# Kernel tuning notes

Measured on AMD Instinct MI355X. Metric: run time of the kernel, lower is better.

The kernel has to match this reference:

```python
import jax, jax.numpy as jnp
import numpy as np

B, T, L, D, H = 4, 8, 197, 512, 8
DK = D // H
SIM_TH = 0.0
N = T * (L - 1)  # 1568 local tokens

def _ln(x, g, b, eps=1e-5):
    x32 = x.astype(jnp.float32)
    m = jnp.mean(x32, axis=-1, keepdims=True)
    v = jnp.mean((x32 - m) ** 2, axis=-1, keepdims=True)
    return (((x32 - m) * jax.lax.rsqrt(v + eps)) * g + b).astype(x.dtype)

def _qgelu(x):
    return x * jax.nn.sigmoid(1.702 * x)

def _mha(x, w_in, b_in, w_out, b_out):
    # torch nn.MultiheadAttention, x: [S, Bt, D] (seq-first)
    S, Bt, _ = x.shape
    qkv = x @ w_in.T + b_in
    q, k, v = jnp.split(qkv, 3, axis=-1)
    q = q.reshape(S, Bt, H, DK); k = k.reshape(S, Bt, H, DK); v = v.reshape(S, Bt, H, DK)
    scores = jnp.einsum('sbhd,tbhd->bhst', q, k) / jnp.sqrt(jnp.asarray(DK, x.dtype))
    p = jax.nn.softmax(scores, axis=-1)
    o = jnp.einsum('bhst,tbhd->sbhd', p, v).reshape(S, Bt, D)
    return o @ w_out.T + b_out

def _resblock(x, ln1g, ln1b, inw, inb, outw, outb, ln2g, ln2b, fcw, fcb, pw, pb):
    x = x + _mha(_ln(x, ln1g, ln1b), inw, inb, outw, outb)
    h = _qgelu(_ln(x, ln2g, ln2b) @ fcw.T + fcb)
    return x + h @ pw.T + pb

def _build_graph(x, g_mask):
    xd = jax.lax.stop_gradient(x)  # matches x.detach()
    xn = xd / jnp.maximum(jnp.linalg.norm(xd, axis=-1, keepdims=True), 1e-12)
    sim = jnp.einsum('bnd,bmd->bnm', xn, xn)
    adj = jnp.where(sim < SIM_TH, 0.0, sim)
    return adj * g_mask  # t != 1 branch

def _graph_attn(x, mask, wq, bq, wk, bk, wv, bv, wo, bo):
    Bb, Nn, _ = x.shape
    def heads(a):
        return a.reshape(Bb, Nn, H, DK).transpose(0, 2, 1, 3)
    Q = heads(x @ wq.T + bq); K = heads(x @ wk.T + bk); V = heads(x @ wv.T + bv)
    scores = jnp.einsum('bhnd,bhmd->bhnm', Q, K) / jnp.sqrt(jnp.asarray(DK, x.dtype))
    m = mask[:, None]  # [b,1,N,N]
    scores = jnp.where(m == 0, -jnp.inf, scores * m)  # scores*mask then masked_fill(mask==0,-inf)
    p = jax.nn.softmax(scores, axis=-1)
    o = jnp.einsum('bhnm,bhmd->bhnd', p, V).transpose(0, 2, 1, 3).reshape(Bb, Nn, D)
    return o @ wo.T + bo

def _forward(x, proj_w, proj_b,
             m_ln1g, m_ln1b, m_inw, m_inb, m_outw, m_outb,
             m_ln2g, m_ln2b, m_fcw, m_fcb, m_pw, m_pb,
             g_wq, g_bq, g_wk, g_bk, g_wv, g_bv, g_wo, g_bo,
             ln1g, ln1b, a_inw, a_inb, a_outw, a_outb,
             ln2g, ln2b, fcw, fcb, pw, pb, g_mask):
    b, t, l, d = x.shape
    x = x @ proj_w.T + proj_b
    glob = x[:, :, 0, :].transpose(1, 0, 2)  # [t,b,d]
    msg = (m_ln1g, m_ln1b, m_inw, m_inb, m_outw, m_outb, m_ln2g, m_ln2b, m_fcw, m_fcb, m_pw, m_pb)
    glob = _resblock(glob, *msg)
    glob = _resblock(glob, *msg)  # message_attn applied twice (shared weights)
    glob = glob.reshape(1, t, b, d)
    loc = x[:, :, 1:, :].reshape(b, t * (l - 1), d)
    gm = _build_graph(loc, g_mask)
    loc = _graph_attn(loc, gm, g_wq, g_bq, g_wk, g_bk, g_wv, g_bv, g_wo, g_bo)
    loc = loc.reshape(b, t, l - 1, d).transpose(2, 1, 0, 3)  # [l-1,t,b,d]
    y = jnp.concatenate([glob, loc], axis=0).reshape(l, t * b, d)
    y = y + _mha(_ln(y, ln1g, ln1b), a_inw, a_inb, a_outw, a_outb)
    y = y + _qgelu(_ln(y, ln2g, ln2b) @ fcw.T + fcb) @ pw.T + pb
    return y.reshape(l, t, b, d).transpose(2, 1, 0, 3)  # [b,t,l,d]

def setup_inputs() -> dict:
    key = jax.random.key(0)
    ks = jax.random.split(key, 64)
    s = 0.02
    def w(i, shape):
        return jax.random.normal(ks[i], shape, jnp.float32) * s
    ones = jnp.ones((D,), jnp.float32); zeros = jnp.zeros((D,), jnp.float32)
    gm = (jax.random.uniform(ks[60], (N, N)) < 0.5).astype(jnp.float32)
    gm = gm.at[jnp.arange(N), jnp.arange(N)].set(1.0)  # keep self-edges so no row is fully masked
    return dict(
        x=jax.random.normal(ks[0], (B, T, L, D), jnp.float32),
        proj_w=w(1, (D, D)), proj_b=jnp.zeros((D,), jnp.float32),
        m_ln1g=ones, m_ln1b=zeros,
        m_inw=w(2, (3 * D, D)), m_inb=jnp.zeros((3 * D,), jnp.float32),
        m_outw=w(3, (D, D)), m_outb=zeros,
        m_ln2g=ones, m_ln2b=zeros,
        m_fcw=w(4, (4 * D, D)), m_fcb=jnp.zeros((4 * D,), jnp.float32),
        m_pw=w(5, (D, 4 * D)), m_pb=zeros,
        g_wq=w(6, (D, D)), g_bq=zeros, g_wk=w(7, (D, D)), g_bk=zeros,
        g_wv=w(8, (D, D)), g_bv=zeros, g_wo=w(9, (D, D)), g_bo=zeros,
        ln1g=ones, ln1b=zeros,
        a_inw=w(10, (3 * D, D)), a_inb=jnp.zeros((3 * D,), jnp.float32),
        a_outw=w(11, (D, D)), a_outb=zeros,
        ln2g=ones, ln2b=zeros,
        fcw=w(12, (4 * D, D)), fcb=jnp.zeros((4 * D,), jnp.float32),
        pw=w(13, (D, 4 * D)), pb=zeros,
        g_mask=gm,
    )

def reference(x, proj_w, proj_b, m_ln1g, m_ln1b, m_inw, m_inb, m_outw, m_outb,
              m_ln2g, m_ln2b, m_fcw, m_fcb, m_pw, m_pb,
              g_wq, g_bq, g_wk, g_bk, g_wv, g_bv, g_wo, g_bo,
              ln1g, ln1b, a_inw, a_inb, a_outw, a_outb,
              ln2g, ln2b, fcw, fcb, pw, pb, g_mask):
    return _forward(x, proj_w, proj_b, m_ln1g, m_ln1b, m_inw, m_inb, m_outw, m_outb,
                    m_ln2g, m_ln2b, m_fcw, m_fcb, m_pw, m_pb,
                    g_wq, g_bq, g_wk, g_bk, g_wv, g_bv, g_wo, g_bo,
                    ln1g, ln1b, a_inw, a_inb, a_outw, a_outb,
                    ln2g, ln2b, fcw, fcb, pw, pb, g_mask)
```

## Files before the change

kernel.cpp:

```cpp
#include <hip/hip_runtime.h>
#include <hip/hip_bf16.h>

typedef unsigned short u16;
typedef __attribute__((ext_vector_type(8))) short bf16x8;
typedef __attribute__((ext_vector_type(4))) float f32x4;

#define FINF __builtin_huge_valf()

static __device__ __forceinline__ float bf2f(u16 v){ union{unsigned u; float f;} c; c.u = ((unsigned)v)<<16; return c.f; }
static __device__ __forceinline__ u16 f2bf(float f){ union{__hip_bfloat16 h; u16 u;} c; c.h = __float2bfloat16(f); return c.u; }
static __device__ __forceinline__ bf16x8 scale8(bf16x8 v, float s){
  bf16x8 o;
  #pragma unroll
  for (int e=0;e<8;e++) o[e] = (short)f2bf(bf2f((u16)v[e])*s);
  return o;
}

static __device__ __forceinline__ void gload16(const void* g, void* l){
  __builtin_amdgcn_global_load_lds(
      (const __attribute__((address_space(1))) void*)g,
      (__attribute__((address_space(3))) void*)l, 16, 0, 0);
}

#define WAIT_VM0()   { asm volatile("s_waitcnt vmcnt(0)" ::: "memory"); __builtin_amdgcn_sched_barrier(0); }
#define BARRIER()    { __builtin_amdgcn_sched_barrier(0); __builtin_amdgcn_s_barrier(); __builtin_amdgcn_sched_barrier(0); }

struct CvtArgs {
  const float* src[14];
  u16* dst[14];
  int n[14];
};
__global__ __launch_bounds__(256) void cvt_multi(CvtArgs a){
  int seg = blockIdx.y;
  const float* s = a.src[seg]; u16* d = a.dst[seg]; int n = a.n[seg];
  for (int i = (blockIdx.x*256 + threadIdx.x)*4; i < n; i += gridDim.x*256*4){
    float4 v = *(const float4*)(s + i);
    ushort4 o = { f2bf(v.x), f2bf(v.y), f2bf(v.z), f2bf(v.w) };
    *(ushort4*)(d + i) = o;
  }
}

__global__ __launch_bounds__(256) void concat_bias(const float* a, const float* b, const float* c, float* o){
  int i = blockIdx.x*256 + threadIdx.x;
  o[i] = i < 512 ? a[i] : (i < 1024 ? b[i-512] : c[i-1024]);
}

template<int BM, int EPI, int MW>
__global__ __launch_bounds__(256,MW) void gemm_nt(
    const u16* __restrict__ A, const u16* __restrict__ Bw,
    const float* __restrict__ bias, const float* aux, void* out,
    int M, int Nn, int K, int ldc, long aBatch, long bBatch, long cBatch)
{
  constexpr int MI = BM/32;
  constexpr int WSPAN = BM/2;
  __shared__ __align__(16) u16 a_lds[2*BM*64];
  __shared__ __align__(16) u16 b_lds[2*128*64];
  const int z = blockIdx.z;
  const u16* Az = A + (long)z*aBatch;
  const u16* Bz = Bw + (long)z*bBatch;
  const int n0 = blockIdx.x*128, m0 = blockIdx.y*BM;
  const int t = threadIdx.x, lane = t & 63, wave = t >> 6;
  const int wr = wave >> 1, wc = wave & 1;
  const int r = lane & 15, kq = lane >> 4;

  const int srow = t >> 3;
  const int scol = ((t&7)*8) ^ ((srow&7)<<3);
  int rowA[MI], rowB[4];
  #pragma unroll
  for (int i=0;i<MI;i++){ int ga = m0 + i*32 + srow; rowA[i] = ga < M ? ga : M-1; }
  #pragma unroll
  for (int i=0;i<4;i++){ int gb = n0 + i*32 + srow; rowB[i] = gb < Nn ? gb : Nn-1; }

  f32x4 acc[MI][4] = {};
  const int nkt = K >> 6;

  auto STAGE = [&](int kt, int buf){
    const long koff = (long)kt*64 + scol;
    #pragma unroll
    for (int i=0;i<MI;i++)
      gload16(Az + (long)rowA[i]*K + koff, (char*)a_lds + buf*(BM*128) + i*4096 + wave*1024);
    #pragma unroll
    for (int i=0;i<4;i++)
      gload16(Bz + (long)rowB[i]*K + koff, (char*)b_lds + buf*16384 + i*4096 + wave*1024);
  };

  STAGE(0,0);
  WAIT_VM0(); BARRIER();
  for (int kt=0; kt<nkt; kt++){
    const int cur = kt&1;
    if (kt+1 < nkt) STAGE(kt+1, cur^1);
    const u16* al = a_lds + cur*BM*64;
    const u16* bl = b_lds + cur*8192;
    #pragma unroll
    for (int kk=0; kk<2; kk++){
      bf16x8 af[MI], bfr[4];
      #pragma unroll
      for (int i=0;i<MI;i++){
        int rw = wr*WSPAN + i*16 + r;
        af[i] = *(const bf16x8*)&al[rw*64 + ((kk*32 + kq*8) ^ ((rw&7)<<3))];
      }
      #pragma unroll
      for (int j=0;j<4;j++){
        int rw = wc*64 + j*16 + r;
        bfr[j] = *(const bf16x8*)&bl[rw*64 + ((kk*32 + kq*8) ^ ((rw&7)<<3))];
      }
      #pragma unroll
      for (int i=0;i<MI;i++)
        #pragma unroll
        for (int j=0;j<4;j++)
          acc[i][j] = __builtin_amdgcn_mfma_f32_16x16x32_bf16(af[i], bfr[j], acc[i][j], 0,0,0);
    }
    WAIT_VM0(); BARRIER();
  }

  #pragma unroll
  for (int i=0;i<MI;i++){
    #pragma unroll
    for (int j=0;j<4;j++){
      int gcol = n0 + wc*64 + j*16 + r;
      if (gcol >= Nn) continue;
      float bv = bias ? bias[gcol] : 0.f;
      #pragma unroll
      for (int rr=0; rr<4; rr++){
        int grow = m0 + wr*WSPAN + i*16 + kq*4 + rr;
        if (grow >= M) continue;
        float v = acc[i][j][rr] + bv;
        if constexpr (EPI==0){
          ((float*)out)[(long)z*cBatch + (long)grow*ldc + gcol] = v;
        } else if constexpr (EPI==1){
          ((u16*)out)[(long)z*cBatch + (long)grow*ldc + gcol] = f2bf(v);
        } else if constexpr (EPI==2){
          long idx = (long)z*cBatch + (long)grow*ldc + gcol;
          ((float*)out)[idx] = aux[idx] + v;
        } else if constexpr (EPI==3){
          float g = v / (1.f + __expf(-1.702f*v));
          ((u16*)out)[(long)z*cBatch + (long)grow*ldc + gcol] = f2bf(g);
        } else if constexpr (EPI==4){
          float adj = v < 0.f ? 0.f : v;
          float gmv = aux[(long)grow*Nn + gcol];
          ((u16*)out)[(long)z*cBatch + (long)grow*ldc + gcol] = f2bf(adj*gmv);
        } else if constexpr (EPI==5){
          int b = grow/1568, n = grow%1568, tt = n/196, lp = n%196;
          int yrow = (1+lp)*32 + tt*4 + b;
          ((float*)out)[(long)yrow*ldc + gcol] = v;
        } else if constexpr (EPI==6){
          long idx = (long)grow*ldc + gcol;
          int l = grow>>5, rb = grow&31, tt = rb>>2, bb = rb&3;
          ((float*)out)[((long)((bb*8+tt)*197) + l)*512 + gcol] = aux[idx] + v;
        }
      }
    }
  }
}

__global__ __launch_bounds__(256) void transpose_v(
    const u16* __restrict__ src, u16* __restrict__ vt,
    int nrows, long zofs, long nofs, int vcol0, int outld)
{
  __shared__ u16 tile[64][66];
  const int t = threadIdx.x;
  const int nt = blockIdx.x, h = blockIdx.y, z = blockIdx.z;
  const int n0 = nt*64;
  const int rlo = t>>3, c0 = (t&7)*8;
  #pragma unroll
  for (int i=0;i<2;i++){
    int nl = i*32 + rlo;
    int n = n0 + nl; int nc = n < nrows ? n : nrows-1;
    const u16* s = src + (long)z*zofs + (long)nc*nofs + vcol0 + h*64 + c0;
    uint4 v = *(const uint4*)s;
    bool dead = n >= nrows;
    #pragma unroll
    for (int e=0;e<8;e++) tile[nl][c0+e] = dead ? (u16)0 : ((const u16*)&v)[e];
  }
  __syncthreads();
  #pragma unroll
  for (int i=0;i<2;i++){
    int d = i*32 + rlo;
    u16 tmp[8];
    #pragma unroll
    for (int e=0;e<8;e++) tmp[e] = tile[c0+e][d];
    int ncol = n0 + c0;
    if (ncol + 8 <= outld){
      u16* dst = vt + ((long)((z*8+h)*64 + d))*outld + ncol;
      *(uint4*)dst = *(uint4*)tmp;
    }
  }
}

template<bool MASKED>
__global__ __launch_bounds__(256,3) void flash4(
    const u16* __restrict__ QKV, const u16* __restrict__ VT,
    const u16* __restrict__ gmask, u16* __restrict__ Out,
    int nq, int nk, int nqb, long qBatch, long qRow,
    long oBatch, long oRow, long gmBatch, int vtld)
{
  __shared__ __align__(16) u16 k_lds[2*4096];
  __shared__ __align__(16) u16 p_lds[4][2][1024];
  int h, z, qb;
  if constexpr (MASKED){
    int id = blockIdx.x;
    int a = id>>6, c = id&7; h = (id>>3)&7;
    int G = a*8 + c;
    if (G >= 4*nqb) return;
    z = G / nqb; qb = G % nqb;
  } else {
    qb = blockIdx.x; h = blockIdx.y; z = blockIdx.z;
  }
  const int t = threadIdx.x, lane = t&63, wave = t>>6;
  const int r = lane&15, kq = lane>>4;
  const u16* Qb = QKV + (long)z*qBatch + h*64;
  const u16* Kb = Qb + 512;
  const u16* Vt = VT + (long)(z*8+h)*64*vtld;
  const int qt0 = qb*128;

  int qi[2], qc[2];
  bf16x8 qf[2][2];
  const u16* Gq[2];
  #pragma unroll
  for (int qt=0; qt<2; qt++){
    qi[qt] = qt0 + qt*64 + wave*16 + r;
    qc[qt] = qi[qt] < nq ? qi[qt] : nq-1;
    const u16* qp = Qb + (long)qc[qt]*qRow + kq*8;
    qf[qt][0] = scale8(*(const bf16x8*)qp, 0.125f);
    qf[qt][1] = scale8(*(const bf16x8*)(qp+32), 0.125f);
    Gq[qt] = MASKED ? (gmask + (long)z*gmBatch + (long)qc[qt]*nk) : nullptr;
  }

  const int srow = t>>3;
  const int scol = ((t&7)*8) ^ ((srow&7)<<3);

  auto stage_k = [&](int kt, int buf){
    #pragma unroll
    for (int i=0;i<2;i++){
      int j = kt*64 + i*32 + srow; if (j > nk-1) j = nk-1;
      gload16(Kb + (long)j*qRow + scol, (char*)k_lds + buf*8192 + i*4096 + wave*1024);
    }
  };

  bf16x8 ONES;
  #pragma unroll
  for (int e=0;e<8;e++) ONES[e] = (short)0x3F80;

  float m_[2] = {-FINF,-FINF};
  f32x4 o_[2][4] = {};  f32x4 l_[2] = {};

  const int nkt = (nk + 63) >> 6;
  stage_k(0,0);
  __syncthreads();
  for (int kt=0; kt<nkt; kt++){
    const int cur = kt&1;
    if (kt+1 < nkt) stage_k(kt+1, cur^1);

    uint4 vfr[2][4];
    #pragma unroll
    for (int c=0;c<2;c++)
      #pragma unroll
      for (int j=0;j<4;j++)
        vfr[c][j] = *(const uint4*)(Vt + (long)(j*16+r)*vtld + kt*64 + c*32 + kq*8);

    const u16* kl = k_lds + cur*4096;
    #pragma unroll
    for (int qt=0; qt<2; qt++){
      ushort4 gv[4];
      if constexpr (MASKED){
        #pragma unroll
        for (int sub=0;sub<4;sub++)
          gv[sub] = *(const ushort4*)(Gq[qt] + kt*64 + sub*16 + kq*4);
      }

      float p[4][4];
      #pragma unroll
      for (int sub=0; sub<4; sub++){
        int rw = sub*16 + r; int sw = (rw&7)<<3;
        bf16x8 kf0 = *(const bf16x8*)&kl[rw*64 + ((kq*8) ^ sw)];
        bf16x8 kf1 = *(const bf16x8*)&kl[rw*64 + ((32 + kq*8) ^ sw)];
        f32x4 sc = {};
        sc = __builtin_amdgcn_mfma_f32_16x16x32_bf16(kf0, qf[qt][0], sc, 0,0,0);
        sc = __builtin_amdgcn_mfma_f32_16x16x32_bf16(kf1, qf[qt][1], sc, 0,0,0);
        #pragma unroll
        for (int rr=0;rr<4;rr++){
          float sv = sc[rr];
          int key = kt*64 + sub*16 + kq*4 + rr;
          if constexpr (MASKED){
            u16 g = ((const u16*)&gv[sub])[rr];
            sv = (g == 0 || key >= nk) ? -FINF : sv * bf2f(g);
          } else {
            if (key >= nk) sv = -FINF;
          }
          p[sub][rr] = sv;
        }
      }

      float mx;
      { float a0 = fmaxf(fmaxf(p[0][0],p[0][1]), fmaxf(p[0][2],p[0][3]));
        float a1 = fmaxf(fmaxf(p[1][0],p[1][1]), fmaxf(p[1][2],p[1][3]));
        float a2 = fmaxf(fmaxf(p[2][0],p[2][1]), fmaxf(p[2][2],p[2][3]));
        float a3 = fmaxf(fmaxf(p[3][0],p[3][1]), fmaxf(p[3][2],p[3][3]));
        mx = fmaxf(fmaxf(a0,a1), fmaxf(a2,a3)); }
      mx = fmaxf(mx, __shfl_xor(mx, 16));
      mx = fmaxf(mx, __shfl_xor(mx, 32));
      float mnew = fmaxf(m_[qt], mx);
      if (__any(mnew > m_[qt])){
        float fac = (m_[qt] == -FINF) ? 0.f : __expf(m_[qt] - mnew);
        #pragma unroll
        for (int j=0;j<4;j++){ o_[qt][j][0]*=fac; o_[qt][j][1]*=fac; o_[qt][j][2]*=fac; o_[qt][j][3]*=fac; }
        l_[qt][0]*=fac; l_[qt][1]*=fac; l_[qt][2]*=fac; l_[qt][3]*=fac;
        m_[qt] = mnew;
      }
      mnew = m_[qt];

      #pragma unroll
      for (int sub=0;sub<4;sub++){
        float e0 = (p[sub][0] == -FINF) ? 0.f : __expf(p[sub][0] - mnew);
        float e1 = (p[sub][1] == -FINF) ? 0.f : __expf(p[sub][1] - mnew);
        float e2 = (p[sub][2] == -FINF) ? 0.f : __expf(p[sub][2] - mnew);
        float e3 = (p[sub][3] == -FINF) ? 0.f : __expf(p[sub][3] - mnew);
        unsigned u0, u1;
        asm volatile("v_cvt_pk_bf16_f32 %0, %1, %2" : "=v"(u0) : "v"(e0), "v"(e1));
        asm volatile("v_cvt_pk_bf16_f32 %0, %1, %2" : "=v"(u1) : "v"(e2), "v"(e3));
        uint2 w; w.x = u0; w.y = u1;
        int idx = r*64 + ((sub*16 + kq*4) ^ ((r&7)<<3));
        *(uint2*)&p_lds[wave][qt][idx] = w;
      }

      #pragma unroll
      for (int c=0;c<2;c++){
        bf16x8 pf = *(const bf16x8*)&p_lds[wave][qt][r*64 + ((c*32 + kq*8) ^ ((r&7)<<3))];
        #pragma unroll
        for (int j=0;j<4;j++){
          bf16x8 vf = *(const bf16x8*)&vfr[c][j];
          o_[qt][j] = __builtin_amdgcn_mfma_f32_16x16x32_bf16(vf, pf, o_[qt][j], 0,0,0);
        }
        l_[qt] = __builtin_amdgcn_mfma_f32_16x16x32_bf16(ONES, pf, l_[qt], 0,0,0);
      }
    }
    __syncthreads();
  }

  #pragma unroll
  for (int qt=0; qt<2; qt++){
    float inv = l_[qt][0] > 0.f ? 1.f/l_[qt][0] : 0.f;
    if (qi[qt] < nq){
      #pragma unroll
      for (int j=0;j<4;j++){
        ushort4 ov = { f2bf(o_[qt][j][0]*inv), f2bf(o_[qt][j][1]*inv),
                       f2bf(o_[qt][j][2]*inv), f2bf(o_[qt][j][3]*inv) };
        *(ushort4*)(Out + (long)z*oBatch + (long)qi[qt]*oRow + h*64 + j*16 + kq*4) = ov;
      }
    }
  }
}

__global__ __launch_bounds__(256) void ln_rows(const float* __restrict__ in,
    const float* __restrict__ g, const float* __restrict__ b, u16* __restrict__ out, int rows)
{
  int wave = threadIdx.x >> 6, lane = threadIdx.x & 63;
  int row = blockIdx.x*4 + wave;
  if (row >= rows) return;
  const float4* x = (const float4*)(in + (long)row*512);
  float4 v0 = x[lane], v1 = x[lane+64];
  float s  = v0.x+v0.y+v0.z+v0.w + v1.x+v1.y+v1.z+v1.w;
  float ss = v0.x*v0.x+v0.y*v0.y+v0.z*v0.z+v0.w*v0.w + v1.x*v1.x+v1.y*v1.y+v1.z*v1.z+v1.w*v1.w;
  #pragma unroll
  for (int d=1; d<64; d<<=1){ s += __shfl_xor(s,d); ss += __shfl_xor(ss,d); }
  float mean = s * (1.f/512.f);
  float var = ss * (1.f/512.f) - mean*mean;
  float rs = rsqrtf(var + 1e-5f);
  const float4* gg = (const float4*)g; const float4* bb = (const float4*)b;
  float4 g0 = gg[lane], g1 = gg[lane+64], b0 = bb[lane], b1 = bb[lane+64];
  u16* o = out + (long)row*512;
  ushort4 o0 = { f2bf((v0.x-mean)*rs*g0.x + b0.x), f2bf((v0.y-mean)*rs*g0.y + b0.y),
                 f2bf((v0.z-mean)*rs*g0.z + b0.z), f2bf((v0.w-mean)*rs*g0.w + b0.w) };
  ushort4 o1 = { f2bf((v1.x-mean)*rs*g1.x + b1.x), f2bf((v1.y-mean)*rs*g1.y + b1.y),
                 f2bf((v1.z-mean)*rs*g1.z + b1.z), f2bf((v1.w-mean)*rs*g1.w + b1.w) };
  *(ushort4*)(o + lane*4) = o0;
  *(ushort4*)(o + 256 + lane*4) = o1;
}

__global__ __launch_bounds__(256) void locprep(const float* __restrict__ y0,
    u16* __restrict__ xn, u16* __restrict__ locb)
{
  int wave = threadIdx.x >> 6, lane = threadIdx.x & 63;
  int rr = blockIdx.x*4 + wave;
  int bb = rr/1568, n = rr%1568, tt = n/196, lp = n%196;
  const float4* x = (const float4*)(y0 + ((long)((bb*8+tt)*197) + 1 + lp)*512);
  float4 v0 = x[lane], v1 = x[lane+64];
  float ss = v0.x*v0.x+v0.y*v0.y+v0.z*v0.z+v0.w*v0.w + v1.x*v1.x+v1.y*v1.y+v1.z*v1.z+v1.w*v1.w;
  #pragma unroll
  for (int d=1; d<64; d<<=1) ss += __shfl_xor(ss,d);
  float sc = 1.f / fmaxf(sqrtf(ss), 1e-12f);
  u16* ox = xn + (long)rr*512;
  u16* ol = locb + (long)rr*512;
  ushort4 a0 = { f2bf(v0.x*sc), f2bf(v0.y*sc), f2bf(v0.z*sc), f2bf(v0.w*sc) };
  ushort4 a1 = { f2bf(v1.x*sc), f2bf(v1.y*sc), f2bf(v1.z*sc), f2bf(v1.w*sc) };
  ushort4 c0 = { f2bf(v0.x), f2bf(v0.y), f2bf(v0.z), f2bf(v0.w) };
  ushort4 c1 = { f2bf(v1.x), f2bf(v1.y), f2bf(v1.z), f2bf(v1.w) };
  *(ushort4*)(ox + lane*4) = a0;  *(ushort4*)(ox + 256 + lane*4) = a1;
  *(ushort4*)(ol + lane*4) = c0;  *(ushort4*)(ol + 256 + lane*4) = c1;
}

__global__ __launch_bounds__(64) void msg_attn(const u16* __restrict__ mqkv, u16* __restrict__ matt){
  __shared__ float q_s[8][64], k_s[8][64], v_s[8][64];
  int bh = blockIdx.x; int bt = bh>>3, h = bh&7;
  int lane = threadIdx.x;
  int row = lane>>3, cc = (lane&7)*8;
  #pragma unroll
  for (int e=0;e<8;e++){
    long base = (long)(row*4 + bt)*1536 + h*64 + cc + e;
    q_s[row][cc+e] = bf2f(mqkv[base]);
    k_s[row][cc+e] = bf2f(mqkv[base + 512]);
    v_s[row][cc+e] = bf2f(mqkv[base + 1024]);
  }
  __syncthreads();
  int q = lane>>3, k = lane&7;
  float s = 0.f;
  #pragma unroll 16
  for (int d=0; d<64; d++) s += q_s[q][d]*k_s[k][d];
  s *= 0.125f;
  float mx = s;
  #pragma unroll
  for (int d=1; d<8; d<<=1) mx = fmaxf(mx, __shfl_xor(mx,d));
  float p = __expf(s - mx), ps = p;
  #pragma unroll
  for (int d=1; d<8; d<<=1) ps += __shfl_xor(ps,d);
  p /= ps;
  for (int d=0; d<64; d++){
    float ov = p * v_s[k][d];
    #pragma unroll
    for (int m=1; m<8; m<<=1) ov += __shfl_xor(ov,m);
    if (k == (d>>3)) matt[(long)(q*4 + bt)*512 + h*64 + d] = f2bf(ov);
  }
}

__global__ __launch_bounds__(256) void gather_glob(const float* __restrict__ y0, float* __restrict__ glob){
  int idx = blockIdx.x*256 + threadIdx.x;
  int orow = idx>>9, d = idx&511;
  int tt = orow>>2, bb = orow&3;
  glob[idx] = y0[((long)(bb*8+tt)*197)*512 + d];
}
__global__ __launch_bounds__(256) void copy32(const float* __restrict__ glob, float* __restrict__ y){
  int idx = blockIdx.x*256 + threadIdx.x;
  y[idx] = glob[idx];
}

extern "C" void kernel_launch(void* const* d_in, const int* in_sizes, int n_in,
                              void* d_out, int out_size, void* d_ws, size_t ws_size,
                              hipStream_t stream)
{
  const float* x      = (const float*)d_in[0];
  const float* proj_w = (const float*)d_in[1];
  const float* proj_b = (const float*)d_in[2];
  const float* m_ln1g = (const float*)d_in[3];
  const float* m_ln1b = (const float*)d_in[4];
  const float* m_inw  = (const float*)d_in[5];
  const float* m_inb  = (const float*)d_in[6];
  const float* m_outw = (const float*)d_in[7];
  const float* m_outb = (const float*)d_in[8];
  const float* m_ln2g = (const float*)d_in[9];
  const float* m_ln2b = (const float*)d_in[10];
  const float* m_fcw  = (const float*)d_in[11];
  const float* m_fcb  = (const float*)d_in[12];
  const float* m_pw   = (const float*)d_in[13];
  const float* m_pb   = (const float*)d_in[14];
  const float* g_wq = (const float*)d_in[15]; const float* g_bq = (const float*)d_in[16];
  const float* g_wk = (const float*)d_in[17]; const float* g_bk = (const float*)d_in[18];
  const float* g_wv = (const float*)d_in[19]; const float* g_bv = (const float*)d_in[20];
  const float* g_wo = (const float*)d_in[21]; const float* g_bo = (const float*)d_in[22];
  const float* ln1g = (const float*)d_in[23]; const float* ln1b = (const float*)d_in[24];
  const float* a_inw = (const float*)d_in[25]; const float* a_inb = (const float*)d_in[26];
  const float* a_outw = (const float*)d_in[27]; const float* a_outb = (const float*)d_in[28];
  const float* ln2g = (const float*)d_in[29]; const float* ln2b = (const float*)d_in[30];
  const float* fcw = (const float*)d_in[31]; const float* fcb = (const float*)d_in[32];
  const float* pw = (const float*)d_in[33]; const float* pb = (const float*)d_in[34];
  const float* g_mask = (const float*)d_in[35];

  if (ws_size < (size_t)99753984) return;

  char* ws = (char*)d_ws;
  u16* WB = (u16*)ws;
  const long WPROJ=0, WMIN=262144, WMOUT=1048576, WMFC=1310720, WMP=2359296,
             WGQ=3407872, WGK=3670016, WGV=3932160, WGO=4194304,
             WAIN=4456448, WAOUT=5242880, WFC=5505024, WP=6553600;
  float* y0   = (float*)(ws + 15204352);
  float* y    = (float*)(ws + 28114944);
  u16* lnbuf  = (u16*)(ws + 41025536);
  u16* vtg    = (u16*)(ws + 41025536);
  u16* locb   = (u16*)(ws + 47480832);
  u16* qkv    = (u16*)(ws + 53903360);
  u16* xb     = (u16*)(ws + 73269248);
  u16* gm     = (u16*)(ws + 73269248);
  u16* vt2    = (u16*)(ws + 73269248);
  u16* hbuf   = (u16*)(ws + 73269248);
  u16* obuf   = (u16*)(ws + 92938240);
  float* glob = (float*)(ws + 99393536);
  u16* mlnb   = (u16*)(ws + 99459072);
  u16* mqkv   = (u16*)(ws + 99491840);
  u16* matt   = (u16*)(ws + 99590144);
  u16* mh     = (u16*)(ws + 99622912);
  float* gbias = (float*)(ws + 99622912);

  CvtArgs ca;
  auto setseg=[&](int i, const float* s, u16* d, int n){ ca.src[i]=s; ca.dst[i]=d; ca.n[i]=n; };
  setseg(0,  x,      xb,       6304*512);
  setseg(1,  proj_w, WB+WPROJ, 262144);
  setseg(2,  m_inw,  WB+WMIN,  786432);
  setseg(3,  m_outw, WB+WMOUT, 262144);
  setseg(4,  m_fcw,  WB+WMFC,  1048576);
  setseg(5,  m_pw,   WB+WMP,   1048576);
  setseg(6,  g_wq,   WB+WGQ,   262144);
  setseg(7,  g_wk,   WB+WGK,   262144);
  setseg(8,  g_wv,   WB+WGV,   262144);
  setseg(9,  g_wo,   WB+WGO,   262144);
  setseg(10, a_inw,  WB+WAIN,  786432);
  setseg(11, a_outw, WB+WAOUT, 262144);
  setseg(12, fcw,    WB+WFC,   1048576);
  setseg(13, pw,     WB+WP,    1048576);
  cvt_multi<<<dim3(128,14), 256, 0, stream>>>(ca);

  gemm_nt<32,0,4><<<dim3(4,197), 256, 0, stream>>>(xb, WB+WPROJ, proj_b, nullptr, y0, 6304,512,512,512, 0,0,0);

  gather_glob<<<64,256,0,stream>>>(y0, glob);

  for (int it=0; it<2; ++it){
    ln_rows<<<8,256,0,stream>>>(glob, m_ln1g, m_ln1b, mlnb, 32);
    gemm_nt<32,1,4><<<dim3(12,1),256,0,stream>>>(mlnb, WB+WMIN, m_inb, nullptr, mqkv, 32,1536,512,1536, 0,0,0);
    msg_attn<<<32,64,0,stream>>>(mqkv, matt);
    gemm_nt<32,2,4><<<dim3(4,1),256,0,stream>>>(matt, WB+WMOUT, m_outb, glob, glob, 32,512,512,512, 0,0,0);
    ln_rows<<<8,256,0,stream>>>(glob, m_ln2g, m_ln2b, mlnb, 32);
    gemm_nt<32,3,4><<<dim3(16,1),256,0,stream>>>(mlnb, WB+WMFC, m_fcb, nullptr, mh, 32,2048,512,2048, 0,0,0);
    gemm_nt<32,2,4><<<dim3(4,1),256,0,stream>>>(mh, WB+WMP, m_pb, glob, glob, 32,512,2048,512, 0,0,0);
  }

  concat_bias<<<6,256,0,stream>>>(g_bq, g_bk, g_bv, gbias);

  locprep<<<1568,256,0,stream>>>(y0, lnbuf, locb);

  gemm_nt<64,4,3><<<dim3(13,25,4),256,0,stream>>>(lnbuf, lnbuf, nullptr, g_mask, gm,
      1568,1568,512,1568, 1568L*512, 1568L*512, 1568L*1568);

  gemm_nt<64,1,3><<<dim3(12,98),256,0,stream>>>(locb, WB+WGQ, gbias, nullptr, qkv, 6272,1536,512,1536, 0,0,0);

  transpose_v<<<dim3(25,8,4),256,0,stream>>>(qkv, vtg, 1568, 1568L*1536, 1536L, 1024, 1568);

  flash4<true><<<448,256,0,stream>>>(qkv, vtg, gm, obuf,
      1568,1568,13, 1568L*1536, 1536, 1568L*512, 512, 1568L*1568, 1568);

  gemm_nt<32,5,4><<<dim3(4,196),256,0,stream>>>(obuf, WB+WGO, g_bo, nullptr, y, 6272,512,512,512, 0,0,0);

  copy32<<<64,256,0,stream>>>(glob, y);

  ln_rows<<<1576,256,0,stream>>>(y, ln1g, ln1b, lnbuf, 6304);
  gemm_nt<64,1,3><<<dim3(12,99),256,0,stream>>>(lnbuf, WB+WAIN, a_inb, nullptr, qkv, 6304,1536,512,1536, 0,0,0);
  transpose_v<<<dim3(4,8,32),256,0,stream>>>(qkv, vt2, 197, 1536L, 32L*1536, 1024, 256);
  flash4<false><<<dim3(2,8,32),256,0,stream>>>(qkv, vt2, nullptr, obuf,
      197,197,2, 1536, 32L*1536, 512, 32L*512, 0, 256);
  gemm_nt<32,2,4><<<dim3(4,197),256,0,stream>>>(obuf, WB+WAOUT, a_outb, y, y, 6304,512,512,512, 0,0,0);

  ln_rows<<<1576,256,0,stream>>>(y, ln2g, ln2b, lnbuf, 6304);
  gemm_nt<64,3,3><<<dim3(16,99),256,0,stream>>>(lnbuf, WB+WFC, fcb, nullptr, hbuf, 6304,2048,512,2048, 0,0,0);
  gemm_nt<32,6,4><<<dim3(4,197),256,0,stream>>>(hbuf, WB+WP, pb, y, (float*)d_out, 6304,512,2048,512, 0,0,0);
}
```

Before: 520.7 us.

## Split masked graph flash attention over two KV halves with combine kernel

The masked graph-attention flash kernel now splits the key/value range into two halves. Each block processes one half and writes unnormalized fp32 partial outputs plus running max and sum to workspace. A new combine kernel merges the two halves with log-sum-exp weighting and writes the bf16 output. This roughly doubles the number of blocks (from 416 active to 832) so the GPU fills better, at the cost of extra fp32 partial traffic and one more kernel launch.

```diff
diff --git a/kernel.cpp b/kernel.cpp
--- a/kernel.cpp
+++ b/kernel.cpp
@@ -187,24 +187,31 @@
   }
 }
 
-template<bool MASKED>
+template<bool MASKED, bool SPLIT>
 __global__ __launch_bounds__(256,3) void flash4(
     const u16* __restrict__ QKV, const u16* __restrict__ VT,
     const u16* __restrict__ gmask, u16* __restrict__ Out,
-    int nq, int nk, int nqb, long qBatch, long qRow,
-    long oBatch, long oRow, long gmBatch, int vtld)
+    float* __restrict__ Op, float* __restrict__ ML,
+    int nq, int nk, int nqb, int kvhalf,
+    long qBatch, long qRow, long oBatch, long oRow, long gmBatch, int vtld)
 {
   __shared__ __align__(16) u16 k_lds[2*4096];
   __shared__ __align__(16) u16 p_lds[4][2][1024];
-  int h, z, qb;
+  int h, z, qb, half = 0, kv0 = 0, kvend;
   if constexpr (MASKED){
     int id = blockIdx.x;
     int a = id>>6, c = id&7; h = (id>>3)&7;
     int G = a*8 + c;
-    if (G >= 4*nqb) return;
-    z = G / nqb; qb = G % nqb;
+    if constexpr (SPLIT){
+      if (G >= 4*nqb*2) return;
+      z = G/(nqb*2); int rem = G%(nqb*2); qb = rem>>1; half = rem&1;
+      kv0 = half*kvhalf; kvend = half ? nk : kvhalf;
+    } else {
+      if (G >= 4*nqb) return;
+      z = G / nqb; qb = G % nqb; kvend = nk;
+    }
   } else {
-    qb = blockIdx.x; h = blockIdx.y; z = blockIdx.z;
+    qb = blockIdx.x; h = blockIdx.y; z = blockIdx.z; kvend = nk;
   }
   const int t = threadIdx.x, lane = t&63, wave = t>>6;
   const int r = lane&15, kq = lane>>4;
@@ -232,7 +239,7 @@
   auto stage_k = [&](int kt, int buf){
     #pragma unroll
     for (int i=0;i<2;i++){
-      int j = kt*64 + i*32 + srow; if (j > nk-1) j = nk-1;
+      int j = kv0 + kt*64 + i*32 + srow; if (j > nk-1) j = nk-1;
       gload16(Kb + (long)j*qRow + scol, (char*)k_lds + buf*8192 + i*4096 + wave*1024);
     }
   };
@@ -244,7 +251,7 @@
   float m_[2] = {-FINF,-FINF};
   f32x4 o_[2][4] = {};  f32x4 l_[2] = {};
 
-  const int nkt = (nk + 63) >> 6;
+  const int nkt = (kvend - kv0 + 63) >> 6;
   stage_k(0,0);
   __syncthreads();
   for (int kt=0; kt<nkt; kt++){
@@ -256,7 +263,7 @@
     for (int c=0;c<2;c++)
       #pragma unroll
       for (int j=0;j<4;j++)
-        vfr[c][j] = *(const uint4*)(Vt + (long)(j*16+r)*vtld + kt*64 + c*32 + kq*8);
+        vfr[c][j] = *(const uint4*)(Vt + (long)(j*16+r)*vtld + kv0 + kt*64 + c*32 + kq*8);
 
     const u16* kl = k_lds + cur*4096;
     #pragma unroll
@@ -265,7 +272,7 @@
       if constexpr (MASKED){
         #pragma unroll
         for (int sub=0;sub<4;sub++)
-          gv[sub] = *(const ushort4*)(Gq[qt] + kt*64 + sub*16 + kq*4);
+          gv[sub] = *(const ushort4*)(Gq[qt] + kv0 + kt*64 + sub*16 + kq*4);
       }
 
       float p[4][4];
@@ -280,12 +287,12 @@
         #pragma unroll
         for (int rr=0;rr<4;rr++){
           float sv = sc[rr];
-          int key = kt*64 + sub*16 + kq*4 + rr;
+          int key = kv0 + kt*64 + sub*16 + kq*4 + rr;
           if constexpr (MASKED){
             u16 g = ((const u16*)&gv[sub])[rr];
-            sv = (g == 0 || key >= nk) ? -FINF : sv * bf2f(g);
+            sv = (g == 0 || key >= kvend) ? -FINF : sv * bf2f(g);
           } else {
-            if (key >= nk) sv = -FINF;
+            if (key >= kvend) sv = -FINF;
           }
           p[sub][rr] = sv;
         }
@@ -339,8 +346,22 @@
 
   #pragma unroll
   for (int qt=0; qt<2; qt++){
-    float inv = l_[qt][0] > 0.f ? 1.f/l_[qt][0] : 0.f;
-    if (qi[qt] < nq){
+    if (qi[qt] >= nq) continue;
+    if constexpr (SPLIT){
+      float* Oph = Op + (long)half*((long)4*nq*512);
+      float* MLh = ML + (long)half*((long)4*8*nq*2);
+      long rowb = ((long)z*nq + qi[qt])*512 + h*64;
+      #pragma unroll
+      for (int j=0;j<4;j++){
+        float4 pv = { o_[qt][j][0], o_[qt][j][1], o_[qt][j][2], o_[qt][j][3] };
+        *(float4*)(Oph + rowb + j*16 + kq*4) = pv;
+      }
+      if (kq == 0){
+        float2 v2 = { m_[qt], l_[qt][0] };
+        *(float2*)(MLh + ((long)(z*8+h)*nq + qi[qt])*2) = v2;
+      }
+    } else {
+      float inv = l_[qt][0] > 0.f ? 1.f/l_[qt][0] : 0.f;
       #pragma unroll
       for (int j=0;j<4;j++){
         ushort4 ov = { f2bf(o_[qt][j][0]*inv), f2bf(o_[qt][j][1]*inv),
@@ -349,6 +370,32 @@
       }
     }
   }
+}
+
+__global__ __launch_bounds__(256) void combine_flash(
+    const float* __restrict__ Op, const float* __restrict__ ML,
+    u16* __restrict__ obuf, int nq)
+{
+  int idx = blockIdx.x*256 + threadIdx.x;
+  int c4 = idx & 127;
+  long zq = idx >> 7;
+  int z = (int)(zq / nq), q = (int)(zq % nq);
+  int h = c4 >> 4;
+  const float* Op1 = Op + (long)4*nq*512;
+  const float* ML1 = ML + (long)4*8*nq*2;
+  long mli = ((long)(z*8+h)*nq + q)*2;
+  float m0 = ML[mli],  l0 = ML[mli+1];
+  float m1 = ML1[mli], l1 = ML1[mli+1];
+  float m = fmaxf(m0, m1);
+  float w0 = (m0 == -FINF) ? 0.f : __expf(m0 - m);
+  float w1 = (m1 == -FINF) ? 0.f : __expf(m1 - m);
+  float l = l0*w0 + l1*w1;
+  float inv = l > 0.f ? 1.f/l : 0.f;
+  float4 p0 = ((const float4*)Op)[idx];
+  float4 p1 = ((const float4*)Op1)[idx];
+  ushort4 o = { f2bf((p0.x*w0 + p1.x*w1)*inv), f2bf((p0.y*w0 + p1.y*w1)*inv),
+                f2bf((p0.z*w0 + p1.z*w1)*inv), f2bf((p0.w*w0 + p1.w*w1)*inv) };
+  ((ushort4*)obuf)[idx] = o;
 }
 
 __global__ __launch_bounds__(256) void ln_rows(const float* __restrict__ in,
@@ -483,9 +530,11 @@
              WAIN=4456448, WAOUT=5242880, WFC=5505024, WP=6553600;
   float* y0   = (float*)(ws + 15204352);
   float* y    = (float*)(ws + 28114944);
+  float* Opar = (float*)(ws + 15204352);
   u16* lnbuf  = (u16*)(ws + 41025536);
   u16* vtg    = (u16*)(ws + 41025536);
   u16* locb   = (u16*)(ws + 47480832);
+  float* MLb  = (float*)(ws + 47480832);
   u16* qkv    = (u16*)(ws + 53903360);
   u16* xb     = (u16*)(ws + 73269248);
   u16* gm     = (u16*)(ws + 73269248);
@@ -542,8 +591,9 @@
 
   transpose_v<<<dim3(25,8,4),256,0,stream>>>(qkv, vtg, 1568, 1568L*1536, 1536L, 1024, 1568);
 
-  flash4<true><<<448,256,0,stream>>>(qkv, vtg, gm, obuf,
-      1568,1568,13, 1568L*1536, 1536, 1568L*512, 512, 1568L*1568, 1568);
+  flash4<true,true><<<832,256,0,stream>>>(qkv, vtg, gm, nullptr, Opar, MLb,
+      1568,1568,13,784, 1568L*1536, 1536, 0, 0, 1568L*1568, 1568);
+  combine_flash<<<3136,256,0,stream>>>(Opar, MLb, obuf, 1568);
 
   gemm_nt<32,5,4><<<dim3(4,196),256,0,stream>>>(obuf, WB+WGO, g_bo, nullptr, y, 6272,512,512,512, 0,0,0);
 
@@ -552,8 +602,8 @@
   ln_rows<<<1576,256,0,stream>>>(y, ln1g, ln1b, lnbuf, 6304);
   gemm_nt<64,1,3><<<dim3(12,99),256,0,stream>>>(lnbuf, WB+WAIN, a_inb, nullptr, qkv, 6304,1536,512,1536, 0,0,0);
   transpose_v<<<dim3(4,8,32),256,0,stream>>>(qkv, vt2, 197, 1536L, 32L*1536, 1024, 256);
-  flash4<false><<<dim3(2,8,32),256,0,stream>>>(qkv, vt2, nullptr, obuf,
-      197,197,2, 1536, 32L*1536, 512, 32L*512, 0, 256);
+  flash4<false,false><<<dim3(2,8,32),256,0,stream>>>(qkv, vt2, nullptr, obuf, nullptr, nullptr,
+      197,197,2,0, 1536, 32L*1536, 512, 32L*512, 0, 256);
   gemm_nt<32,2,4><<<dim3(4,197),256,0,stream>>>(obuf, WB+WAOUT, a_outb, y, y, 6304,512,512,512, 0,0,0);
 
   ln_rows<<<1576,256,0,stream>>>(y, ln2g, ln2b, lnbuf, 6304);
```

Measured after the change: 532.0 us. 1.02x slower.
